# Kernel tuning notes

Hardware: AMD Instinct MI355X
Metric: run time of the kernel (lower is better)

Reference implementation:

```python
import jax, jax.numpy as jnp
import numpy as np

N = 100000      # nodes
E = 800000      # edges (avg degree 8)
D_IN = 128      # in_channels
HEADS = 8
C = 16          # out_channels per head (heads*C = 128 output dim)
NEG_SLOPE = 0.2  # PyG GATConv default leaky_relu slope


def setup_inputs() -> dict:
    key = jax.random.key(0)
    ks = jax.random.split(key, 12)
    s = 1.0 / np.sqrt(D_IN)
    x = jax.random.normal(ks[0], (N, D_IN), jnp.float32)
    ei = jax.random.randint(ks[1], (2, E), 0, N, jnp.int32)
    return {
        "x": x,
        "ei": ei,
        # conv_in GATConv params
        "W_in": jax.random.normal(ks[2], (D_IN, HEADS * C), jnp.float32) * s,
        "a_src_in": jax.random.normal(ks[3], (HEADS, C), jnp.float32) * s,
        "a_dst_in": jax.random.normal(ks[4], (HEADS, C), jnp.float32) * s,
        "b_in": jnp.zeros((HEADS * C,), jnp.float32),
        # conv_out GATConv params (applied to flipped edges)
        "W_out": jax.random.normal(ks[5], (D_IN, HEADS * C), jnp.float32) * s,
        "a_src_out": jax.random.normal(ks[6], (HEADS, C), jnp.float32) * s,
        "a_dst_out": jax.random.normal(ks[7], (HEADS, C), jnp.float32) * s,
        "b_out": jnp.zeros((HEADS * C,), jnp.float32),
    }


def _gat_conv(x, src, dst, W, a_src, a_dst, b):
    # h: [N, H, C] projected node features
    h = (x @ W).reshape(N, HEADS, C)
    # per-node attention logits [N, H]
    alpha_src = jnp.einsum("nhc,hc->nh", h, a_src)
    alpha_dst = jnp.einsum("nhc,hc->nh", h, a_dst)
    # per-edge logits, message flows src -> dst; softmax grouped by dst
    logits = jax.nn.leaky_relu(alpha_src[src] + alpha_dst[dst], NEG_SLOPE)  # [E, H]
    seg_max = jax.ops.segment_max(logits, dst, num_segments=N)              # [N, H]
    ex = jnp.exp(logits - seg_max[dst])
    denom = jax.ops.segment_sum(ex, dst, num_segments=N)                    # [N, H]
    coef = ex / denom[dst]                                                  # [E, H]
    msg = h[src] * coef[:, :, None]                                         # [E, H, C]
    out = jax.ops.segment_sum(msg, dst, num_segments=N)                     # [N, H, C]
    return out.reshape(N, HEADS * C) + b


def reference(x, ei, W_in, a_src_in, a_dst_in, b_in, W_out, a_src_out, a_dst_out, b_out):
    src, dst = ei[0], ei[1]
    # DirSeq: conv_in on (src->dst), conv_out on flipped edges (dst->src)
    x_in = _gat_conv(x, src, dst, W_in, a_src_in, a_dst_in, b_in)
    x_out = _gat_conv(x, dst, src, W_out, a_src_out, a_dst_out, b_out)
    return x_in + x_out
```

## Files before the change

### kernel.cpp

```cpp
#include <hip/hip_runtime.h>

#define N_NODES 100000
#define N_EDGES 800000
#define NEG 0.2f
#define PB_SHIFT 8
#define PB_NODES 256
#define N_PBKT ((N_NODES + PB_NODES - 1) / PB_NODES)
#define TILE_E 4096
#define EPT 16
#define PREP_BLOCKS ((N_NODES * 128 / 4 + 255) / 256)
#define HIST_BLOCKS 192

typedef __attribute__((ext_vector_type(8))) short bf16x8;
typedef __attribute__((ext_vector_type(4))) float f32x4;

__device__ inline unsigned short f2bf(float f) {
    unsigned u = __float_as_uint(f);
    u += 0x7fffu + ((u >> 16) & 1u);
    return (unsigned short)(u >> 16);
}
__device__ inline float bf2f_lo(unsigned u) { return __uint_as_float(u << 16); }
__device__ inline float bf2f_hi(unsigned u) { return __uint_as_float(u & 0xffff0000u); }

__global__ __launch_bounds__(256) void prep_w_kernel(
    const float* __restrict__ W_in, const float* __restrict__ W_out,
    const float* __restrict__ as_in, const float* __restrict__ ad_in,
    const float* __restrict__ as_out, const float* __restrict__ ad_out,
    unsigned short* __restrict__ Wf, int* __restrict__ bcnt,
    int* __restrict__ adj_in, int* __restrict__ adj_out)
{
    const int t = blockIdx.x * 256 + threadIdx.x;
    if (t < 2 * N_PBKT) bcnt[t] = 0;
    if (t < 8) { adj_in[N_EDGES + t] = 0; adj_out[N_EDGES + t] = 0; }
    if (t >= 2 * 4 * 9 * 64) return;
    const int lane = t & 63;
    const int rest = t >> 6;
    const int ct  = rest % 9;
    const int kb  = (rest / 9) & 3;
    const int dir = rest / 36;
    const float* W  = dir ? W_out  : W_in;
    const float* as = dir ? as_out : as_in;
    const float* ad = dir ? ad_out : ad_in;
    const int m16 = lane & 15, quad = lane >> 4;

    bf16x8 o;
#pragma unroll
    for (int j = 0; j < 8; ++j) {
        const int k = kb * 32 + quad * 8 + j;
        float v;
        if (ct < 8) {
            v = W[k * 128 + ct * 16 + m16];
        } else {
            const float* av = (m16 < 8) ? as : ad;
            const int hh = m16 & 7;
            v = 0.f;
            for (int c = 0; c < 16; ++c)
                v += W[k * 128 + hh * 16 + c] * av[hh * 16 + c];
        }
        o[j] = (short)f2bf(v);
    }
    *(bf16x8*)&Wf[(long long)t * 8] = o;
}

__global__ __launch_bounds__(256) void prep_hist_kernel(
    const float* __restrict__ x, unsigned short* __restrict__ x_bf,
    const int* __restrict__ ei, int* __restrict__ bcnt)
{
    const int tid = threadIdx.x;
    if (blockIdx.x < PREP_BLOCKS) {
        const int i = (blockIdx.x * 256 + tid) * 4;
        if (i >= N_NODES * 128) return;
        const float4 v = *(const float4*)&x[i];
        ushort4 o;
        o.x = f2bf(v.x); o.y = f2bf(v.y); o.z = f2bf(v.z); o.w = f2bf(v.w);
        *(ushort4*)&x_bf[i] = o;
        return;
    }
    __shared__ int bh[2 * N_PBKT];
    for (int i = tid; i < 2 * N_PBKT; i += 256) bh[i] = 0;
    __syncthreads();
    const int hb = blockIdx.x - PREP_BLOCKS;
    for (int e = hb * 256 + tid; e < N_EDGES; e += HIST_BLOCKS * 256) {
        const int s = ei[e];
        const int t = ei[N_EDGES + e];
        atomicAdd(&bh[t >> PB_SHIFT], 1);
        atomicAdd(&bh[N_PBKT + (s >> PB_SHIFT)], 1);
    }
    __syncthreads();
    for (int i = tid; i < 2 * N_PBKT; i += 256) {
        const int v = bh[i];
        if (v) atomicAdd(&bcnt[i], v);
    }
}

__global__ __launch_bounds__(256) void gemm_kernel(
    const unsigned short* __restrict__ x_bf,
    const unsigned short* __restrict__ Wf,
    unsigned short* __restrict__ h_in, unsigned short* __restrict__ h_out,
    float* __restrict__ asrc_in, float* __restrict__ adst_in,
    float* __restrict__ asrc_out, float* __restrict__ adst_out)
{
    const int dir = blockIdx.y;
    unsigned short* h = dir ? h_out : h_in;
    float* asrc = dir ? asrc_out : asrc_in;
    float* adst = dir ? adst_out : adst_in;

    const int tid  = threadIdx.x;
    const int lane = tid & 63;
    const int wave = tid >> 6;
    const int m16  = lane & 15;
    const int quad = lane >> 4;
    const int rbase = blockIdx.x * 128 + wave * 32;

    f32x4 acc[2][8];
    f32x4 acc_a[2];
#pragma unroll
    for (int rt = 0; rt < 2; ++rt) {
        acc_a[rt] = f32x4{0.f, 0.f, 0.f, 0.f};
#pragma unroll
        for (int ct = 0; ct < 8; ++ct)
            acc[rt][ct] = f32x4{0.f, 0.f, 0.f, 0.f};
    }

    const unsigned short* wf = Wf + (long long)dir * 4 * 9 * 64 * 8;

#pragma unroll
    for (int kb = 0; kb < 4; ++kb) {
        const int k0 = kb * 32 + quad * 8;
        bf16x8 a[2];
#pragma unroll
        for (int rt = 0; rt < 2; ++rt) {
            int r = rbase + rt * 16 + m16;
            r = r < N_NODES ? r : N_NODES - 1;
            a[rt] = *(const bf16x8*)&x_bf[(long long)r * 128 + k0];
        }
#pragma unroll
        for (int ct = 0; ct < 9; ++ct) {
            const bf16x8 b = *(const bf16x8*)&wf[(long long)((kb * 9 + ct) * 64 + lane) * 8];
            if (ct < 8) {
                acc[0][ct] = __builtin_amdgcn_mfma_f32_16x16x32_bf16(a[0], b, acc[0][ct], 0, 0, 0);
                acc[1][ct] = __builtin_amdgcn_mfma_f32_16x16x32_bf16(a[1], b, acc[1][ct], 0, 0, 0);
            } else {
                acc_a[0] = __builtin_amdgcn_mfma_f32_16x16x32_bf16(a[0], b, acc_a[0], 0, 0, 0);
                acc_a[1] = __builtin_amdgcn_mfma_f32_16x16x32_bf16(a[1], b, acc_a[1], 0, 0, 0);
            }
        }
    }

#pragma unroll
    for (int rt = 0; rt < 2; ++rt) {
#pragma unroll
        for (int r = 0; r < 4; ++r) {
            const int row = rbase + rt * 16 + quad * 4 + r;
            if (row < N_NODES) {
                unsigned short* hp = &h[(long long)row * 128 + m16];
#pragma unroll
                for (int ct = 0; ct < 8; ++ct)
                    hp[ct * 16] = f2bf(acc[rt][ct][r]);
                const float av = acc_a[rt][r];
                if (m16 < 8) asrc[row * 8 + m16] = av;
                else         adst[row * 8 + (m16 - 8)] = av;
            }
        }
    }
}

__global__ __launch_bounds__(512) void bucket_scan_kernel(
    const int* __restrict__ bcnt,
    int* __restrict__ boffs0, int* __restrict__ boffs1,
    int* __restrict__ gcur,
    int* __restrict__ offs_in, int* __restrict__ offs_out)
{
    const int dir = blockIdx.x;
    const int* c = bcnt + dir * N_PBKT;
    int* bo = dir ? boffs1 : boffs0;
    int* gc = gcur + dir * N_PBKT;

    __shared__ int sm[512];
    const int tid = threadIdx.x;
    const int v = (tid < N_PBKT) ? c[tid] : 0;
    sm[tid] = v;
    __syncthreads();
#pragma unroll
    for (int off = 1; off < 512; off <<= 1) {
        int t = (tid >= off) ? sm[tid - off] : 0;
        __syncthreads();
        sm[tid] += t;
        __syncthreads();
    }
    if (tid < N_PBKT) {
        const int excl = sm[tid] - v;
        bo[tid] = excl;
        gc[tid] = excl;
    }
    if (tid == N_PBKT - 1) bo[N_PBKT] = sm[tid];
    if (tid == 0) (dir ? offs_out : offs_in)[N_NODES] = N_EDGES;
}

__global__ __launch_bounds__(256) void partition_kernel(
    const int* __restrict__ ei, int* __restrict__ gcur,
    int* __restrict__ binned0, int* __restrict__ binned1)
{
    __shared__ int hist0[N_PBKT];
    __shared__ int curs0[N_PBKT];
    __shared__ int hist1[N_PBKT];
    __shared__ int curs1[N_PBKT];
    const int tid = threadIdx.x;
    for (int i = tid; i < N_PBKT; i += 256) { hist0[i] = 0; hist1[i] = 0; }
    __syncthreads();

    const int e0 = blockIdx.x * TILE_E;
    int sv[EPT], tv[EPT];
#pragma unroll
    for (int i = 0; i < EPT; ++i) {
        const int e = e0 + i * 256 + tid;
        if (e < N_EDGES) {
            sv[i] = ei[e];
            tv[i] = ei[N_EDGES + e];
            atomicAdd(&hist0[tv[i] >> PB_SHIFT], 1);
            atomicAdd(&hist1[sv[i] >> PB_SHIFT], 1);
        } else {
            sv[i] = -1; tv[i] = 0;
        }
    }
    __syncthreads();
    for (int b = tid; b < N_PBKT; b += 256) {
        int c = hist0[b];
        curs0[b] = c ? atomicAdd(&gcur[b], c) : 0;
        c = hist1[b];
        curs1[b] = c ? atomicAdd(&gcur[N_PBKT + b], c) : 0;
    }
    __syncthreads();
#pragma unroll
    for (int i = 0; i < EPT; ++i) {
        if (sv[i] >= 0) {
            int pos = atomicAdd(&curs0[tv[i] >> PB_SHIFT], 1);
            binned0[pos] = (sv[i] << 8) | (tv[i] & (PB_NODES - 1));
            pos = atomicAdd(&curs1[sv[i] >> PB_SHIFT], 1);
            binned1[pos] = (tv[i] << 8) | (sv[i] & (PB_NODES - 1));
        }
    }
}

__global__ __launch_bounds__(256) void place_kernel(
    const int* __restrict__ binned0, const int* __restrict__ binned1,
    const int* __restrict__ boffs0, const int* __restrict__ boffs1,
    int* __restrict__ adj_in, int* __restrict__ adj_out,
    int* __restrict__ offs_in, int* __restrict__ offs_out)
{
    const int b   = blockIdx.x;
    const int dir = blockIdx.y;
    const int* bp = dir ? binned1 : binned0;
    const int* bo = dir ? boffs1  : boffs0;
    int* adj  = dir ? adj_out  : adj_in;
    int* offs = dir ? offs_out : offs_in;

    const int base = b << PB_SHIFT;
    const int beg = bo[b], end = bo[b + 1];
    const int tid = threadIdx.x;

    __shared__ int cnt[PB_NODES];
    __shared__ int sc[PB_NODES];
    __shared__ int cur[PB_NODES];

    cnt[tid] = 0;
    __syncthreads();
    for (int p = beg + tid; p < end; p += 256)
        atomicAdd(&cnt[bp[p] & (PB_NODES - 1)], 1);
    __syncthreads();
    const int v = cnt[tid];
    sc[tid] = v;
    __syncthreads();
#pragma unroll
    for (int off = 1; off < PB_NODES; off <<= 1) {
        int t = (tid >= off) ? sc[tid - off] : 0;
        __syncthreads();
        sc[tid] += t;
        __syncthreads();
    }
    const int excl = beg + sc[tid] - v;
    cur[tid] = excl;
    const int node = base + tid;
    if (node < N_NODES) offs[node] = excl;
    __syncthreads();
    for (int p = beg + tid; p < end; p += 256) {
        const int pk = bp[p];
        adj[atomicAdd(&cur[pk & (PB_NODES - 1)], 1)] = pk >> 8;
    }
}

__global__ __launch_bounds__(256) void gather_kernel(
    const int* __restrict__ offs_in, const int* __restrict__ adj_in,
    const int* __restrict__ offs_out, const int* __restrict__ adj_out,
    const unsigned short* __restrict__ h_in, const unsigned short* __restrict__ h_out,
    const float* __restrict__ asrc_in, const float* __restrict__ adst_in,
    const float* __restrict__ asrc_out, const float* __restrict__ adst_out,
    const float* __restrict__ b_in, const float* __restrict__ b_out,
    float* __restrict__ out)
{
    int n = (blockIdx.x * 256 + threadIdx.x) >> 6;
    if (n >= N_NODES) return;
    n = __builtin_amdgcn_readfirstlane(n);
    const int lane = threadIdx.x & 63;
    const int c0 = lane * 2;
    const int hh = lane >> 3;
    const int g8 = lane & 7;
    const int grpbase = lane & 56;

    float acc0 = b_in[c0] + b_out[c0];
    float acc1 = b_in[c0 + 1] + b_out[c0 + 1];

#define DIR_BLOCK(OFFS, ADJ, HX, ASRC, ADST)                                   \
    {                                                                          \
        const int beg = OFFS[n], end = OFFS[n + 1];                            \
        if (end > beg) {                                                       \
            const float ad = ADST[n * 8 + hh];                                 \
            float num0 = 0.f, num1 = 0.f, den = 0.f;                           \
            for (int p = beg; p < end; p += 8) {                               \
                const int q = p + g8;                                          \
                const int nbv = ADJ[q];                 \
                float l = ASRC[nbv * 8 + hh] + ad;                             \
                l = l > 0.f ? l : NEG * l;                                     \
                float w = __expf(l);                                           \
                w = (q < end) ? w : 0.f;                                       \
                den += w;                                                      \
                _Pragma("unroll")                                              \
                for (int g = 0; g < 8; ++g) {                                  \
                    const int nb = ADJ[p + g];           \
                    const float w_g = __shfl(w, grpbase + g, 64);              \
                    const unsigned hv = *(const unsigned*)&HX[(long long)nb * 128 + c0]; \
                    num0 += w_g * bf2f_lo(hv);                                 \
                    num1 += w_g * bf2f_hi(hv);                                 \
                }                                                              \
            }                                                                  \
            den += __shfl_xor(den, 1, 64);                                     \
            den += __shfl_xor(den, 2, 64);                                     \
            den += __shfl_xor(den, 4, 64);                                     \
            const float rden = 1.f / den;                                      \
            acc0 += num0 * rden;                                               \
            acc1 += num1 * rden;                                               \
        }                                                                      \
    }

    DIR_BLOCK(offs_in, adj_in, h_in, asrc_in, adst_in)
    DIR_BLOCK(offs_out, adj_out, h_out, asrc_out, adst_out)
#undef DIR_BLOCK

    *(float2*)&out[(long long)n * 128 + c0] = float2{acc0, acc1};
}

extern "C" void kernel_launch(void* const* d_in, const int* in_sizes, int n_in,
                              void* d_out, int out_size, void* d_ws, size_t ws_size,
                              hipStream_t stream) {
    const float* x      = (const float*)d_in[0];
    const int*   ei     = (const int*)  d_in[1];
    const float* W_in   = (const float*)d_in[2];
    const float* as_in  = (const float*)d_in[3];
    const float* ad_in  = (const float*)d_in[4];
    const float* b_in   = (const float*)d_in[5];
    const float* W_out  = (const float*)d_in[6];
    const float* as_out = (const float*)d_in[7];
    const float* ad_out = (const float*)d_in[8];
    const float* b_out  = (const float*)d_in[9];
    float* out = (float*)d_out;

    char* ws = (char*)d_ws;
    const long long NH = (long long)N_NODES * 128;
    unsigned short* x_bf  = (unsigned short*)ws;    ws += NH * 2;
    unsigned short* h_in  = (unsigned short*)ws;    ws += NH * 2;
    unsigned short* h_out = (unsigned short*)ws;    ws += NH * 2;
    unsigned short* Wf    = (unsigned short*)ws;    ws += 2LL * 4 * 9 * 64 * 8 * 2;
    float* asrc_in   = (float*)ws;                  ws += N_NODES * 8 * 4;
    float* adst_in   = (float*)ws;                  ws += N_NODES * 8 * 4;
    float* asrc_out  = (float*)ws;                  ws += N_NODES * 8 * 4;
    float* adst_out  = (float*)ws;                  ws += N_NODES * 8 * 4;
    int* binned0     = (int*)ws;                    ws += (long long)N_EDGES * 4;
    int* binned1     = (int*)ws;                    ws += (long long)N_EDGES * 4;
    int* adj_in      = (int*)ws;                    ws += (N_EDGES + 8) * 4;
    int* adj_out     = (int*)ws;                    ws += (N_EDGES + 8) * 4;
    int* offs_in     = (int*)ws;                    ws += (N_NODES + 1) * 4;
    int* offs_out    = (int*)ws;                    ws += (N_NODES + 1) * 4;
    int* bcnt        = (int*)ws;                    ws += 2 * N_PBKT * 4;
    int* boffs0      = (int*)ws;                    ws += (N_PBKT + 1) * 4;
    int* boffs1      = (int*)ws;                    ws += (N_PBKT + 1) * 4;
    int* gcur        = (int*)ws;                    ws += 2 * N_PBKT * 4;

    prep_w_kernel<<<(2 * 4 * 9 * 64 + 255) / 256, 256, 0, stream>>>(
        W_in, W_out, as_in, ad_in, as_out, ad_out, Wf, bcnt, adj_in, adj_out);
    prep_hist_kernel<<<PREP_BLOCKS + HIST_BLOCKS, 256, 0, stream>>>(
        x, x_bf, ei, bcnt);

    dim3 gemm_grid((N_NODES + 127) / 128, 2);
    gemm_kernel<<<gemm_grid, 256, 0, stream>>>(
        x_bf, Wf, h_in, h_out, asrc_in, adst_in, asrc_out, adst_out);

    bucket_scan_kernel<<<2, 512, 0, stream>>>(
        bcnt, boffs0, boffs1, gcur, offs_in, offs_out);
    partition_kernel<<<(N_EDGES + TILE_E - 1) / TILE_E, 256, 0, stream>>>(
        ei, gcur, binned0, binned1);
    place_kernel<<<dim3(N_PBKT, 2), 256, 0, stream>>>(
        binned0, binned1, boffs0, boffs1, adj_in, adj_out, offs_in, offs_out);

    gather_kernel<<<(N_NODES * 64 + 255) / 256, 256, 0, stream>>>(
        offs_in, adj_in, offs_out, adj_out, h_in, h_out,
        asrc_in, adst_in, asrc_out, adst_out, b_in, b_out, out);
}
```

Baseline: 294.5 us.

## Interleave in/out direction gathers in aggregation loop and shrink edge tile size

```diff
diff --git a/kernel.cpp b/kernel.cpp
--- a/kernel.cpp
+++ b/kernel.cpp
@@ -6,8 +6,8 @@
 #define PB_SHIFT 8
 #define PB_NODES 256
 #define N_PBKT ((N_NODES + PB_NODES - 1) / PB_NODES)
-#define TILE_E 4096
-#define EPT 16
+#define TILE_E 1024
+#define EPT 4
 #define PREP_BLOCKS ((N_NODES * 128 / 4 + 255) / 256)
 #define HIST_BLOCKS 192
 
@@ -310,41 +310,64 @@
     float acc0 = b_in[c0] + b_out[c0];
     float acc1 = b_in[c0 + 1] + b_out[c0 + 1];
 
-#define DIR_BLOCK(OFFS, ADJ, HX, ASRC, ADST)                                   \
+    const int beg0 = offs_in[n],  end0 = offs_in[n + 1];
+    const int beg1 = offs_out[n], end1 = offs_out[n + 1];
+    const float ad0 = adst_in[n * 8 + hh];
+    const float ad1 = adst_out[n * 8 + hh];
+
+    float n00 = 0.f, n01 = 0.f, den0 = 0.f;
+    float n10 = 0.f, n11 = 0.f, den1 = 0.f;
+    int p0 = beg0, p1 = beg1;
+
+#define GRP(ADJ, ASRC, AD, HX, P, END, DEN, NU0, NU1)                          \
     {                                                                          \
-        const int beg = OFFS[n], end = OFFS[n + 1];                            \
-        if (end > beg) {                                                       \
-            const float ad = ADST[n * 8 + hh];                                 \
-            float num0 = 0.f, num1 = 0.f, den = 0.f;                           \
-            for (int p = beg; p < end; p += 8) {                               \
-                const int q = p + g8;                                          \
-                const int nbv = ADJ[q];                 \
-                float l = ASRC[nbv * 8 + hh] + ad;                             \
-                l = l > 0.f ? l : NEG * l;                                     \
-                float w = __expf(l);                                           \
-                w = (q < end) ? w : 0.f;                                       \
-                den += w;                                                      \
-                _Pragma("unroll")                                              \
-                for (int g = 0; g < 8; ++g) {                                  \
-                    const int nb = ADJ[p + g];           \
-                    const float w_g = __shfl(w, grpbase + g, 64);              \
-                    const unsigned hv = *(const unsigned*)&HX[(long long)nb * 128 + c0]; \
-                    num0 += w_g * bf2f_lo(hv);                                 \
-                    num1 += w_g * bf2f_hi(hv);                                 \
-                }                                                              \
-            }                                                                  \
-            den += __shfl_xor(den, 1, 64);                                     \
-            den += __shfl_xor(den, 2, 64);                                     \
-            den += __shfl_xor(den, 4, 64);                                     \
-            const float rden = 1.f / den;                                      \
-            acc0 += num0 * rden;                                               \
-            acc1 += num1 * rden;                                               \
+        const int nbv = ADJ[P + g8];                    \
+        float l = ASRC[nbv * 8 + hh] + AD;                                     \
+        l = l > 0.f ? l : NEG * l;                                             \
+        float w = __expf(l);                                                   \
+        w = (P + g8 < END) ? w : 0.f;                                          \
+        DEN += w;                                                              \
+        _Pragma("unroll")                                                      \
+        for (int g = 0; g < 8; ++g) {                                          \
+            const int nb = ADJ[P + g];                   \
+            const float w_g = __shfl(w, grpbase + g, 64);                      \
+            const unsigned hv = *(const unsigned*)&HX[(long long)nb * 128 + c0]; \
+            NU0 += w_g * bf2f_lo(hv);                                          \
+            NU1 += w_g * bf2f_hi(hv);                                          \
         }                                                                      \
     }
 
-    DIR_BLOCK(offs_in, adj_in, h_in, asrc_in, adst_in)
-    DIR_BLOCK(offs_out, adj_out, h_out, asrc_out, adst_out)
-#undef DIR_BLOCK
+    while (p0 < end0 && p1 < end1) {
+        GRP(adj_in,  asrc_in,  ad0, h_in,  p0, end0, den0, n00, n01)
+        GRP(adj_out, asrc_out, ad1, h_out, p1, end1, den1, n10, n11)
+        p0 += 8; p1 += 8;
+    }
+    while (p0 < end0) {
+        GRP(adj_in,  asrc_in,  ad0, h_in,  p0, end0, den0, n00, n01)
+        p0 += 8;
+    }
+    while (p1 < end1) {
+        GRP(adj_out, asrc_out, ad1, h_out, p1, end1, den1, n10, n11)
+        p1 += 8;
+    }
+#undef GRP
+
+    if (end0 > beg0) {
+        den0 += __shfl_xor(den0, 1, 64);
+        den0 += __shfl_xor(den0, 2, 64);
+        den0 += __shfl_xor(den0, 4, 64);
+        const float r = 1.f / den0;
+        acc0 += n00 * r;
+        acc1 += n01 * r;
+    }
+    if (end1 > beg1) {
+        den1 += __shfl_xor(den1, 1, 64);
+        den1 += __shfl_xor(den1, 2, 64);
+        den1 += __shfl_xor(den1, 4, 64);
+        const float r = 1.f / den1;
+        acc0 += n10 * r;
+        acc1 += n11 * r;
+    }
 
     *(float2*)&out[(long long)n * 128 + c0] = float2{acc0, acc1};
 }
```

Result: slower. 317.2 us (+7.7%).

## Build CSR via per-node degree atomics and direct scatter instead of bucket partition

Applied to the files above, without the earlier changes.

```diff
diff --git a/kernel.cpp b/kernel.cpp
--- a/kernel.cpp
+++ b/kernel.cpp
@@ -6,10 +6,10 @@
 #define PB_SHIFT 8
 #define PB_NODES 256
 #define N_PBKT ((N_NODES + PB_NODES - 1) / PB_NODES)
-#define TILE_E 4096
-#define EPT 16
+#define NDEG (N_PBKT * 256)
 #define PREP_BLOCKS ((N_NODES * 128 / 4 + 255) / 256)
 #define HIST_BLOCKS 192
+#define SCAT_TILE 1024
 
 typedef __attribute__((ext_vector_type(8))) short bf16x8;
 typedef __attribute__((ext_vector_type(4))) float f32x4;
@@ -26,11 +26,12 @@
     const float* __restrict__ W_in, const float* __restrict__ W_out,
     const float* __restrict__ as_in, const float* __restrict__ ad_in,
     const float* __restrict__ as_out, const float* __restrict__ ad_out,
-    unsigned short* __restrict__ Wf, int* __restrict__ bcnt,
+    unsigned short* __restrict__ Wf,
+    int* __restrict__ deg0, int* __restrict__ deg1,
     int* __restrict__ adj_in, int* __restrict__ adj_out)
 {
     const int t = blockIdx.x * 256 + threadIdx.x;
-    if (t < 2 * N_PBKT) bcnt[t] = 0;
+    if (t < NDEG) { deg0[t] = 0; deg1[t] = 0; }
     if (t < 8) { adj_in[N_EDGES + t] = 0; adj_out[N_EDGES + t] = 0; }
     if (t >= 2 * 4 * 9 * 64) return;
     const int lane = t & 63;
@@ -64,7 +65,8 @@
 
 __global__ __launch_bounds__(256) void prep_hist_kernel(
     const float* __restrict__ x, unsigned short* __restrict__ x_bf,
-    const int* __restrict__ ei, int* __restrict__ bcnt)
+    const int* __restrict__ ei,
+    int* __restrict__ deg0, int* __restrict__ deg1)
 {
     const int tid = threadIdx.x;
     if (blockIdx.x < PREP_BLOCKS) {
@@ -76,20 +78,12 @@
         *(ushort4*)&x_bf[i] = o;
         return;
     }
-    __shared__ int bh[2 * N_PBKT];
-    for (int i = tid; i < 2 * N_PBKT; i += 256) bh[i] = 0;
-    __syncthreads();
     const int hb = blockIdx.x - PREP_BLOCKS;
     for (int e = hb * 256 + tid; e < N_EDGES; e += HIST_BLOCKS * 256) {
         const int s = ei[e];
         const int t = ei[N_EDGES + e];
-        atomicAdd(&bh[t >> PB_SHIFT], 1);
-        atomicAdd(&bh[N_PBKT + (s >> PB_SHIFT)], 1);
-    }
-    __syncthreads();
-    for (int i = tid; i < 2 * N_PBKT; i += 256) {
-        const int v = bh[i];
-        if (v) atomicAdd(&bcnt[i], v);
+        atomicAdd(&deg0[t], 1);
+        atomicAdd(&deg1[s], 1);
     }
 }
 
@@ -165,16 +159,34 @@
     }
 }
 
+__global__ __launch_bounds__(256) void bsum_kernel(
+    const int* __restrict__ deg0, const int* __restrict__ deg1,
+    int* __restrict__ bsum)
+{
+    const int dir = blockIdx.y;
+    const int* deg = dir ? deg1 : deg0;
+    __shared__ int sm[256];
+    const int tid = threadIdx.x;
+    sm[tid] = deg[blockIdx.x * 256 + tid];
+    __syncthreads();
+#pragma unroll
+    for (int off = 1; off < 256; off <<= 1) {
+        int t = (tid >= off) ? sm[tid - off] : 0;
+        __syncthreads();
+        sm[tid] += t;
+        __syncthreads();
+    }
+    if (tid == 255) bsum[dir * N_PBKT + blockIdx.x] = sm[255];
+}
+
 __global__ __launch_bounds__(512) void bucket_scan_kernel(
-    const int* __restrict__ bcnt,
+    const int* __restrict__ bsum,
     int* __restrict__ boffs0, int* __restrict__ boffs1,
-    int* __restrict__ gcur,
     int* __restrict__ offs_in, int* __restrict__ offs_out)
 {
     const int dir = blockIdx.x;
-    const int* c = bcnt + dir * N_PBKT;
+    const int* c = bsum + dir * N_PBKT;
     int* bo = dir ? boffs1 : boffs0;
-    int* gc = gcur + dir * N_PBKT;
 
     __shared__ int sm[512];
     const int tid = threadIdx.x;
@@ -188,104 +200,55 @@
         sm[tid] += t;
         __syncthreads();
     }
-    if (tid < N_PBKT) {
-        const int excl = sm[tid] - v;
-        bo[tid] = excl;
-        gc[tid] = excl;
-    }
-    if (tid == N_PBKT - 1) bo[N_PBKT] = sm[tid];
+    if (tid < N_PBKT) bo[tid] = sm[tid] - v;
     if (tid == 0) (dir ? offs_out : offs_in)[N_NODES] = N_EDGES;
 }
 
-__global__ __launch_bounds__(256) void partition_kernel(
-    const int* __restrict__ ei, int* __restrict__ gcur,
-    int* __restrict__ binned0, int* __restrict__ binned1)
-{
-    __shared__ int hist0[N_PBKT];
-    __shared__ int curs0[N_PBKT];
-    __shared__ int hist1[N_PBKT];
-    __shared__ int curs1[N_PBKT];
-    const int tid = threadIdx.x;
-    for (int i = tid; i < N_PBKT; i += 256) { hist0[i] = 0; hist1[i] = 0; }
+__global__ __launch_bounds__(256) void fixup_kernel(
+    const int* __restrict__ deg0, const int* __restrict__ deg1,
+    const int* __restrict__ boffs0, const int* __restrict__ boffs1,
+    int* __restrict__ offs_in, int* __restrict__ offs_out,
+    int* __restrict__ cur0, int* __restrict__ cur1)
+{
+    const int dir = blockIdx.y;
+    const int* deg = dir ? deg1 : deg0;
+    const int* bo  = dir ? boffs1 : boffs0;
+    int* offs = dir ? offs_out : offs_in;
+    int* cur  = dir ? cur1 : cur0;
+
+    __shared__ int sm[256];
+    const int tid = threadIdx.x;
+    const int node = blockIdx.x * 256 + tid;
+    const int v = deg[node];
+    sm[tid] = v;
     __syncthreads();
-
-    const int e0 = blockIdx.x * TILE_E;
-    int sv[EPT], tv[EPT];
-#pragma unroll
-    for (int i = 0; i < EPT; ++i) {
+#pragma unroll
+    for (int off = 1; off < 256; off <<= 1) {
+        int t = (tid >= off) ? sm[tid - off] : 0;
+        __syncthreads();
+        sm[tid] += t;
+        __syncthreads();
+    }
+    const int excl = bo[blockIdx.x] + sm[tid] - v;
+    if (node < N_NODES) { offs[node] = excl; cur[node] = excl; }
+}
+
+__global__ __launch_bounds__(256) void scatter_kernel(
+    const int* __restrict__ ei,
+    int* __restrict__ cur0, int* __restrict__ cur1,
+    int* __restrict__ adj_in, int* __restrict__ adj_out)
+{
+    const int tid = threadIdx.x;
+    const int e0 = blockIdx.x * SCAT_TILE;
+#pragma unroll
+    for (int i = 0; i < SCAT_TILE / 256; ++i) {
         const int e = e0 + i * 256 + tid;
         if (e < N_EDGES) {
-            sv[i] = ei[e];
-            tv[i] = ei[N_EDGES + e];
-            atomicAdd(&hist0[tv[i] >> PB_SHIFT], 1);
-            atomicAdd(&hist1[sv[i] >> PB_SHIFT], 1);
-        } else {
-            sv[i] = -1; tv[i] = 0;
-        }
-    }
-    __syncthreads();
-    for (int b = tid; b < N_PBKT; b += 256) {
-        int c = hist0[b];
-        curs0[b] = c ? atomicAdd(&gcur[b], c) : 0;
-        c = hist1[b];
-        curs1[b] = c ? atomicAdd(&gcur[N_PBKT + b], c) : 0;
-    }
-    __syncthreads();
-#pragma unroll
-    for (int i = 0; i < EPT; ++i) {
-        if (sv[i] >= 0) {
-            int pos = atomicAdd(&curs0[tv[i] >> PB_SHIFT], 1);
-            binned0[pos] = (sv[i] << 8) | (tv[i] & (PB_NODES - 1));
-            pos = atomicAdd(&curs1[sv[i] >> PB_SHIFT], 1);
-            binned1[pos] = (tv[i] << 8) | (sv[i] & (PB_NODES - 1));
-        }
-    }
-}
-
-__global__ __launch_bounds__(256) void place_kernel(
-    const int* __restrict__ binned0, const int* __restrict__ binned1,
-    const int* __restrict__ boffs0, const int* __restrict__ boffs1,
-    int* __restrict__ adj_in, int* __restrict__ adj_out,
-    int* __restrict__ offs_in, int* __restrict__ offs_out)
-{
-    const int b   = blockIdx.x;
-    const int dir = blockIdx.y;
-    const int* bp = dir ? binned1 : binned0;
-    const int* bo = dir ? boffs1  : boffs0;
-    int* adj  = dir ? adj_out  : adj_in;
-    int* offs = dir ? offs_out : offs_in;
-
-    const int base = b << PB_SHIFT;
-    const int beg = bo[b], end = bo[b + 1];
-    const int tid = threadIdx.x;
-
-    __shared__ int cnt[PB_NODES];
-    __shared__ int sc[PB_NODES];
-    __shared__ int cur[PB_NODES];
-
-    cnt[tid] = 0;
-    __syncthreads();
-    for (int p = beg + tid; p < end; p += 256)
-        atomicAdd(&cnt[bp[p] & (PB_NODES - 1)], 1);
-    __syncthreads();
-    const int v = cnt[tid];
-    sc[tid] = v;
-    __syncthreads();
-#pragma unroll
-    for (int off = 1; off < PB_NODES; off <<= 1) {
-        int t = (tid >= off) ? sc[tid - off] : 0;
-        __syncthreads();
-        sc[tid] += t;
-        __syncthreads();
-    }
-    const int excl = beg + sc[tid] - v;
-    cur[tid] = excl;
-    const int node = base + tid;
-    if (node < N_NODES) offs[node] = excl;
-    __syncthreads();
-    for (int p = beg + tid; p < end; p += 256) {
-        const int pk = bp[p];
-        adj[atomicAdd(&cur[pk & (PB_NODES - 1)], 1)] = pk >> 8;
+            const int s = ei[e];
+            const int t = ei[N_EDGES + e];
+            adj_in[atomicAdd(&cur0[t], 1)] = s;
+            adj_out[atomicAdd(&cur1[s], 1)] = t;
+        }
     }
 }
 
@@ -374,32 +337,34 @@
     float* adst_in   = (float*)ws;                  ws += N_NODES * 8 * 4;
     float* asrc_out  = (float*)ws;                  ws += N_NODES * 8 * 4;
     float* adst_out  = (float*)ws;                  ws += N_NODES * 8 * 4;
-    int* binned0     = (int*)ws;                    ws += (long long)N_EDGES * 4;
-    int* binned1     = (int*)ws;                    ws += (long long)N_EDGES * 4;
     int* adj_in      = (int*)ws;                    ws += (N_EDGES + 8) * 4;
     int* adj_out     = (int*)ws;                    ws += (N_EDGES + 8) * 4;
     int* offs_in     = (int*)ws;                    ws += (N_NODES + 1) * 4;
     int* offs_out    = (int*)ws;                    ws += (N_NODES + 1) * 4;
-    int* bcnt        = (int*)ws;                    ws += 2 * N_PBKT * 4;
+    int* deg0        = (int*)ws;                    ws += NDEG * 4;
+    int* deg1        = (int*)ws;                    ws += NDEG * 4;
+    int* cur0        = (int*)ws;                    ws += NDEG * 4;
+    int* cur1        = (int*)ws;                    ws += NDEG * 4;
+    int* bsum        = (int*)ws;                    ws += 2 * N_PBKT * 4;
     int* boffs0      = (int*)ws;                    ws += (N_PBKT + 1) * 4;
     int* boffs1      = (int*)ws;                    ws += (N_PBKT + 1) * 4;
-    int* gcur        = (int*)ws;                    ws += 2 * N_PBKT * 4;
-
-    prep_w_kernel<<<(2 * 4 * 9 * 64 + 255) / 256, 256, 0, stream>>>(
-        W_in, W_out, as_in, ad_in, as_out, ad_out, Wf, bcnt, adj_in, adj_out);
+
+    prep_w_kernel<<<(NDEG + 255) / 256, 256, 0, stream>>>(
+        W_in, W_out, as_in, ad_in, as_out, ad_out, Wf, deg0, deg1, adj_in, adj_out);
     prep_hist_kernel<<<PREP_BLOCKS + HIST_BLOCKS, 256, 0, stream>>>(
-        x, x_bf, ei, bcnt);
+        x, x_bf, ei, deg0, deg1);
 
     dim3 gemm_grid((N_NODES + 127) / 128, 2);
     gemm_kernel<<<gemm_grid, 256, 0, stream>>>(
         x_bf, Wf, h_in, h_out, asrc_in, adst_in, asrc_out, adst_out);
 
+    bsum_kernel<<<dim3(N_PBKT, 2), 256, 0, stream>>>(deg0, deg1, bsum);
     bucket_scan_kernel<<<2, 512, 0, stream>>>(
-        bcnt, boffs0, boffs1, gcur, offs_in, offs_out);
-    partition_kernel<<<(N_EDGES + TILE_E - 1) / TILE_E, 256, 0, stream>>>(
-        ei, gcur, binned0, binned1);
-    place_kernel<<<dim3(N_PBKT, 2), 256, 0, stream>>>(
-        binned0, binned1, boffs0, boffs1, adj_in, adj_out, offs_in, offs_out);
+        bsum, boffs0, boffs1, offs_in, offs_out);
+    fixup_kernel<<<dim3(N_PBKT, 2), 256, 0, stream>>>(
+        deg0, deg1, boffs0, boffs1, offs_in, offs_out, cur0, cur1);
+    scatter_kernel<<<(N_EDGES + SCAT_TILE - 1) / SCAT_TILE, 256, 0, stream>>>(
+        ei, cur0, cur1, adj_in, adj_out);
 
     gather_kernel<<<(N_NODES * 64 + 255) / 256, 256, 0, stream>>>(
         offs_in, adj_in, offs_out, adj_out, h_in, h_out,
```

New measurement: 473.7 us. 60.9% more time.

## Fuse bf16 conversion of x into GEMM and use LDS broadcast for edge weights

Applied to the files above, without the earlier changes.

```diff
diff --git a/kernel.cpp b/kernel.cpp
--- a/kernel.cpp
+++ b/kernel.cpp
@@ -8,7 +8,6 @@
 #define N_PBKT ((N_NODES + PB_NODES - 1) / PB_NODES)
 #define TILE_E 4096
 #define EPT 16
-#define PREP_BLOCKS ((N_NODES * 128 / 4 + 255) / 256)
 #define HIST_BLOCKS 192
 
 typedef __attribute__((ext_vector_type(8))) short bf16x8;
@@ -62,25 +61,14 @@
     *(bf16x8*)&Wf[(long long)t * 8] = o;
 }
 
-__global__ __launch_bounds__(256) void prep_hist_kernel(
-    const float* __restrict__ x, unsigned short* __restrict__ x_bf,
+__global__ __launch_bounds__(256) void hist_kernel(
     const int* __restrict__ ei, int* __restrict__ bcnt)
 {
     const int tid = threadIdx.x;
-    if (blockIdx.x < PREP_BLOCKS) {
-        const int i = (blockIdx.x * 256 + tid) * 4;
-        if (i >= N_NODES * 128) return;
-        const float4 v = *(const float4*)&x[i];
-        ushort4 o;
-        o.x = f2bf(v.x); o.y = f2bf(v.y); o.z = f2bf(v.z); o.w = f2bf(v.w);
-        *(ushort4*)&x_bf[i] = o;
-        return;
-    }
     __shared__ int bh[2 * N_PBKT];
     for (int i = tid; i < 2 * N_PBKT; i += 256) bh[i] = 0;
     __syncthreads();
-    const int hb = blockIdx.x - PREP_BLOCKS;
-    for (int e = hb * 256 + tid; e < N_EDGES; e += HIST_BLOCKS * 256) {
+    for (int e = blockIdx.x * 256 + tid; e < N_EDGES; e += HIST_BLOCKS * 256) {
         const int s = ei[e];
         const int t = ei[N_EDGES + e];
         atomicAdd(&bh[t >> PB_SHIFT], 1);
@@ -94,7 +82,7 @@
 }
 
 __global__ __launch_bounds__(256) void gemm_kernel(
-    const unsigned short* __restrict__ x_bf,
+    const float* __restrict__ x,
     const unsigned short* __restrict__ Wf,
     unsigned short* __restrict__ h_in, unsigned short* __restrict__ h_out,
     float* __restrict__ asrc_in, float* __restrict__ adst_in,
@@ -132,7 +120,12 @@
         for (int rt = 0; rt < 2; ++rt) {
             int r = rbase + rt * 16 + m16;
             r = r < N_NODES ? r : N_NODES - 1;
-            a[rt] = *(const bf16x8*)&x_bf[(long long)r * 128 + k0];
+            const float4 v0 = *(const float4*)&x[(long long)r * 128 + k0];
+            const float4 v1 = *(const float4*)&x[(long long)r * 128 + k0 + 4];
+            a[rt][0] = (short)f2bf(v0.x); a[rt][1] = (short)f2bf(v0.y);
+            a[rt][2] = (short)f2bf(v0.z); a[rt][3] = (short)f2bf(v0.w);
+            a[rt][4] = (short)f2bf(v1.x); a[rt][5] = (short)f2bf(v1.y);
+            a[rt][6] = (short)f2bf(v1.z); a[rt][7] = (short)f2bf(v1.w);
         }
 #pragma unroll
         for (int ct = 0; ct < 9; ++ct) {
@@ -302,10 +295,13 @@
     if (n >= N_NODES) return;
     n = __builtin_amdgcn_readfirstlane(n);
     const int lane = threadIdx.x & 63;
+    const int wave = threadIdx.x >> 6;
     const int c0 = lane * 2;
     const int hh = lane >> 3;
     const int g8 = lane & 7;
-    const int grpbase = lane & 56;
+
+    __shared__ __align__(16) float swbuf[4][64];
+    float* sw = swbuf[wave];
 
     float acc0 = b_in[c0] + b_out[c0];
     float acc1 = b_in[c0 + 1] + b_out[c0 + 1];
@@ -324,10 +320,15 @@
                 float w = __expf(l);                                           \
                 w = (q < end) ? w : 0.f;                                       \
                 den += w;                                                      \
+                sw[hh * 8 + g8] = w;                                           \
+                __builtin_amdgcn_wave_barrier();                               \
+                const f32x4 w03 = *(const f32x4*)&sw[hh * 8];                  \
+                const f32x4 w47 = *(const f32x4*)&sw[hh * 8 + 4];              \
+                __builtin_amdgcn_wave_barrier();                               \
                 _Pragma("unroll")                                              \
                 for (int g = 0; g < 8; ++g) {                                  \
                     const int nb = ADJ[p + g];           \
-                    const float w_g = __shfl(w, grpbase + g, 64);              \
+                    const float w_g = (g < 4) ? w03[g & 3] : w47[g & 3];       \
                     const unsigned hv = *(const unsigned*)&HX[(long long)nb * 128 + c0]; \
                     num0 += w_g * bf2f_lo(hv);                                 \
                     num1 += w_g * bf2f_hi(hv);                                 \
@@ -366,7 +367,6 @@
 
     char* ws = (char*)d_ws;
     const long long NH = (long long)N_NODES * 128;
-    unsigned short* x_bf  = (unsigned short*)ws;    ws += NH * 2;
     unsigned short* h_in  = (unsigned short*)ws;    ws += NH * 2;
     unsigned short* h_out = (unsigned short*)ws;    ws += NH * 2;
     unsigned short* Wf    = (unsigned short*)ws;    ws += 2LL * 4 * 9 * 64 * 8 * 2;
@@ -387,12 +387,11 @@
 
     prep_w_kernel<<<(2 * 4 * 9 * 64 + 255) / 256, 256, 0, stream>>>(
         W_in, W_out, as_in, ad_in, as_out, ad_out, Wf, bcnt, adj_in, adj_out);
-    prep_hist_kernel<<<PREP_BLOCKS + HIST_BLOCKS, 256, 0, stream>>>(
-        x, x_bf, ei, bcnt);
+    hist_kernel<<<HIST_BLOCKS, 256, 0, stream>>>(ei, bcnt);
 
     dim3 gemm_grid((N_NODES + 127) / 128, 2);
     gemm_kernel<<<gemm_grid, 256, 0, stream>>>(
-        x_bf, Wf, h_in, h_out, asrc_in, adst_in, asrc_out, adst_out);
+        x, Wf, h_in, h_out, asrc_in, adst_in, asrc_out, adst_out);
 
     bucket_scan_kernel<<<2, 512, 0, stream>>>(
         bcnt, boffs0, boffs1, gcur, offs_in, offs_out);
```

Result: faster. 280.8 us (-4.6%).
